# Kernel optimization log

Measured on AMD Instinct MI355X. Metric: run time of the kernel, lower is better.

The kernel has to match this reference:

```python
import jax, jax.numpy as jnp
import numpy as np

B, T, LD, PD, W, NL = 2048, 256, 32, 8, 64, 3
TH, CH = LD * 2, W * 2  # token/channel mixing hidden dims (expansion=2)


def setup_inputs() -> dict:
    key = jax.random.key(0)
    ks = jax.random.split(key, 12)
    n = lambda k, s, sc=0.02: jax.random.normal(k, s, jnp.float32) * sc
    return {
        "phys": jax.random.normal(ks[0], (B, T, PD), jnp.float32),
        "latents": jax.random.uniform(ks[1], (B, LD), jnp.float32),
        "pos_emb": n(ks[2], (1, LD, W)),
        "tokW": n(ks[3], (1, W)), "tokb": jnp.zeros((W,), jnp.float32),
        "physW1": n(ks[4], (PD, W)), "physb1": jnp.zeros((W,), jnp.float32),
        "physW2": n(ks[5], (W, W)), "physb2": jnp.zeros((W,), jnp.float32),
        "tn_g": jnp.ones((NL, W), jnp.float32), "tn_b": jnp.zeros((NL, W), jnp.float32),
        "tiW": n(ks[6], (NL, LD, TH)), "tib": jnp.zeros((NL, TH), jnp.float32),
        "toW": n(ks[7], (NL, TH, LD)), "tob": jnp.zeros((NL, LD), jnp.float32),
        "cn_g": jnp.ones((NL, W), jnp.float32), "cn_b": jnp.zeros((NL, W), jnp.float32),
        "ciW": n(ks[8], (NL, W, CH)), "cib": jnp.zeros((NL, CH), jnp.float32),
        "coW": n(ks[9], (NL, CH, W)), "cob": jnp.zeros((NL, W), jnp.float32),
        "hn_g": jnp.ones((W,), jnp.float32), "hn_b": jnp.zeros((W,), jnp.float32),
        "headW": n(ks[10], (W, 1), 0.0002),  # 0.02 init * 0.01 scaling from torch
        "headb": jnp.zeros((1,), jnp.float32),
    }


def _ln(x, g, b):
    m = jnp.mean(x, -1, keepdims=True)
    v = jnp.mean((x - m) ** 2, -1, keepdims=True)
    return (x - m) * jax.lax.rsqrt(v + 1e-5) * g + b


def reference(phys, latents, pos_emb, tokW, tokb, physW1, physb1, physW2, physb2,
              tn_g, tn_b, tiW, tib, toW, tob, cn_g, cn_b, ciW, cib, coW, cob,
              hn_g, hn_b, headW, headb):
    gelu = lambda x: jax.nn.gelu(x, approximate=False)  # torch nn.GELU default (exact)

    def step(current, phys_t):
        # token_projection of current[..., None]: Linear(1, W)
        tokens = current[:, :, None] * tokW[0] + tokb  # [B, LD, W]
        p = gelu(phys_t @ physW1 + physb1) @ physW2 + physb2  # [B, W]
        tokens = tokens + p[:, None, :] + pos_emb
        for i in range(NL):
            # token mixing: LN over width, mix across latent tokens
            mt = jnp.swapaxes(_ln(tokens, tn_g[i], tn_b[i]), 1, 2)  # [B, W, LD]
            mt = gelu(mt @ tiW[i] + tib[i]) @ toW[i] + tob[i]       # [B, W, LD]
            tokens = tokens + jnp.swapaxes(mt, 1, 2)
            # channel mixing over width
            mc = _ln(tokens, cn_g[i], cn_b[i])
            tokens = tokens + (gelu(mc @ ciW[i] + cib[i]) @ coW[i] + cob[i])
        delta = (_ln(tokens, hn_g, hn_b) @ headW + headb)[..., 0]  # [B, LD]
        new = jnp.clip(current + delta, 0.0, 1.0)
        return new, new

    _, outs = jax.lax.scan(step, latents, jnp.swapaxes(phys, 0, 1))  # [T, B, LD]
    return jnp.swapaxes(outs, 0, 1)  # [B, T, LD]
```

## Files before the change

kernel.cpp:

```cpp
#include <hip/hip_runtime.h>
#include <math.h>


namespace {
constexpr int Tt = 256, NL = 3;

typedef float    f32x4 __attribute__((ext_vector_type(4)));
typedef _Float16 half2 __attribute__((ext_vector_type(2)));
typedef _Float16 h16x4 __attribute__((ext_vector_type(4)));
typedef _Float16 h16x8 __attribute__((ext_vector_type(8)));

#define MFMA32(a, b, c) __builtin_amdgcn_mfma_f32_16x16x32_f16((a), (b), (c), 0, 0, 0)
#define MFMA16(a, b, c) __builtin_amdgcn_mfma_f32_16x16x16f16((a), (b), (c), 0, 0, 0)

__device__ __forceinline__ half2 h2c(float v) { return (half2)((_Float16)v); }
__device__ __forceinline__ f32x4 f4s(float v) { return (f32x4)v; }
__device__ __forceinline__ half2 pkrtz(float a, float b) {
    return __builtin_bit_cast(half2, __builtin_amdgcn_cvt_pkrtz(a, b));
}
__device__ __forceinline__ void st4h(short* p, half2 a, half2 b) {
    uint2 v;
    v.x = __builtin_bit_cast(unsigned int, a);
    v.y = __builtin_bit_cast(unsigned int, b);
    *(uint2*)p = v;
}
__device__ __forceinline__ h16x4 h4(half2 a, half2 b) {
    h16x4 v; v[0] = a[0]; v[1] = a[1]; v[2] = b[0]; v[3] = b[1]; return v;
}
__device__ __forceinline__ half2 gelu_pk(half2 x) {
    half2 tc = __builtin_elementwise_min(__builtin_elementwise_max(x, h2c(-3.0f)), h2c(3.0f));
    half2 s = (tc * tc) * h2c(0.125f);
    half2 p = s * h2c(0.1455169f) + h2c(-0.446340f);
    p = s * p + h2c(0.604927f);
    p = s * p + h2c(-0.529702f);
    p = s * p + h2c(0.3989423f);
    return x * (h2c(0.5f) + tc * p);
}
__device__ __forceinline__ float gelu_f(float x) {
    float tc = fminf(fmaxf(x, -3.f), 3.f);
    float s = tc * tc;
    float p = fmaf(s, 3.55266e-5f, -8.71758e-4f);
    p = fmaf(s, p, 9.45198e-3f);
    p = fmaf(s, p, -6.62128e-2f);
    p = fmaf(s, p, 0.3989423f);
    return x * fmaf(tc, p, 0.5f);
}
__device__ __forceinline__ float rowsum16(float x) {
    x += __builtin_bit_cast(float, __builtin_amdgcn_update_dpp(0, __builtin_bit_cast(int, x), 0x121, 0xf, 0xf, false));
    x += __builtin_bit_cast(float, __builtin_amdgcn_update_dpp(0, __builtin_bit_cast(int, x), 0x122, 0xf, 0xf, false));
    x += __builtin_bit_cast(float, __builtin_amdgcn_update_dpp(0, __builtin_bit_cast(int, x), 0x124, 0xf, 0xf, false));
    x += __builtin_bit_cast(float, __builtin_amdgcn_update_dpp(0, __builtin_bit_cast(int, x), 0x128, 0xf, 0xf, false));
    return x;
}
__device__ __forceinline__ short f2h(float x) {
    return __builtin_bit_cast(short, (_Float16)x);
}

__global__ void lno_prep(const float* __restrict__ tiW, const float* __restrict__ toW,
                         const float* __restrict__ ciW, const float* __restrict__ coW,
                         const float* __restrict__ physW2, short* __restrict__ wsf) {
    int id = blockIdx.x * 256 + threadIdx.x;
    if (id < 6144) {
        int e = id & 255, tile = id >> 8;
        int lane = e >> 2, j = e & 3;
        int q = lane >> 4, cc = lane & 15;
        int kc = tile & 1, u = (tile >> 1) & 3, il = tile >> 3;
        wsf[id] = f2h(tiW[il * 2048 + (16 * kc + 4 * q + j) * 64 + 16 * u + cc]);
    } else if (id < 12288) {
        int t = id - 6144;
        int e = t & 255, tile = t >> 8;
        int lane = e >> 2, j = e & 3;
        int q = lane >> 4, cc = lane & 15;
        int kc = tile & 3, mt = (tile >> 2) & 1, il = tile >> 3;
        wsf[id] = f2h(toW[il * 2048 + (16 * kc + 4 * q + j) * 32 + 16 * mt + cc]);
    } else if (id < 36864) {
        int t = id - 12288;
        int j = t & 7, lane = (t >> 3) & 63, g = t >> 9;
        int il = g >> 4, mtc = (g >> 1) & 7, ks = g & 1;
        int m = mtc * 16 + (lane & 15), k = ks * 32 + (lane >> 4) * 8 + j;
        wsf[id] = f2h(ciW[il * 8192 + k * 128 + m]);
    } else if (id < 61440) {
        int t = id - 36864;
        int j = t & 7, lane = (t >> 3) & 63, g = t >> 9;
        int il = g >> 4, nt = (g >> 2) & 3, ks = g & 3;
        int n = nt * 16 + (lane & 15), k = ks * 32 + (lane >> 4) * 8 + j;
        wsf[id] = f2h(coW[il * 8192 + k * 64 + n]);
    } else if (id < 65536) {
        int t = id - 61440;
        int w = t >> 6, k = t & 63;
        ((float*)(wsf + 61440))[t] = physW2[k * 64 + w];
    }
}

__global__ void lno_phys(const float* __restrict__ phys, const float* __restrict__ physW1,
                         const float* __restrict__ physb1, const float* __restrict__ physW2,
                         const float* __restrict__ physb2, short* __restrict__ pout) {
    __shared__ float hsh[4][64];
    const int lane = threadIdx.x & 63, wv = threadIdx.x >> 6;
    const size_t bt = (size_t)blockIdx.x * 4 + wv;
    const float* pt = phys + bt * 8;
    float4 px0 = *(const float4*)pt, px1 = *(const float4*)(pt + 4);
    float a = physb1[lane];
    a = fmaf(px0.x, physW1[0 * 64 + lane], a);
    a = fmaf(px0.y, physW1[1 * 64 + lane], a);
    a = fmaf(px0.z, physW1[2 * 64 + lane], a);
    a = fmaf(px0.w, physW1[3 * 64 + lane], a);
    a = fmaf(px1.x, physW1[4 * 64 + lane], a);
    a = fmaf(px1.y, physW1[5 * 64 + lane], a);
    a = fmaf(px1.z, physW1[6 * 64 + lane], a);
    a = fmaf(px1.w, physW1[7 * 64 + lane], a);
    hsh[wv][lane] = gelu_f(a);
    float acc = physb2[lane];
#pragma unroll
    for (int k = 0; k < 64; ++k) acc = fmaf(hsh[wv][k], physW2[k * 64 + lane], acc);
    pout[bt * 64 + (lane & 15) * 4 + (lane >> 4)] = f2h(acc);
}

__global__ __launch_bounds__(512, 1) void lno_scan(
    const float* __restrict__ latents, const float* __restrict__ pos_emb,
    const float* __restrict__ tokW,    const float* __restrict__ tokb,
    const float* __restrict__ tn_g,    const float* __restrict__ tn_b,
    const float* __restrict__ tib,     const float* __restrict__ tob,
    const float* __restrict__ cn_g,    const float* __restrict__ cn_b,
    const float* __restrict__ cib,     const float* __restrict__ cob,
    const float* __restrict__ hn_g,    const float* __restrict__ hn_b,
    const float* __restrict__ headW,   const float* __restrict__ headb,
    const short* __restrict__ wsf,     const short* pbuf, float* out)
{
    __shared__ __align__(16) short wAll[61440];
    __shared__ __align__(16) short scr[8][2048];
    __shared__ __align__(16) float biasL[1632];

    const int tid = threadIdx.x, lane = tid & 63, wv = tid >> 6;
    const int q = lane >> 4, c = lane & 15;
    const int b = blockIdx.x * 8 + wv;
    short* sc = scr[wv];

    const short* A1L = wAll;
    const short* A2L = wAll + 6144;
    const short* A3L = wAll + 12288;
    const short* B4L = wAll + 36864;

    {
        const unsigned int* src = (const unsigned int*)wsf;
#pragma unroll
        for (int i = 0; i < 15; ++i) {
            const int cid = wv * 15 + i;
            __builtin_amdgcn_global_load_lds(src + cid * 256 + lane * 4,
                                             (unsigned int*)&wAll[cid * 512], 16, 0, 0);
        }
    }
    for (int i = tid; i < 192; i += 512) {
        biasL[i] = tib[i];
        biasL[672 + i]  = tn_g[i];
        biasL[864 + i]  = tn_b[i];
        biasL[1056 + i] = cn_g[i];
        biasL[1248 + i] = cn_b[i];
        biasL[1440 + i] = cob[i];
    }
    for (int i = tid; i < 96;  i += 512) biasL[192 + i] = tob[i];
    for (int i = tid; i < 384; i += 512) biasL[288 + i] = cib[i];

    float tokw_r[4], gh_r[4];
#pragma unroll
    for (int nt = 0; nt < 4; ++nt) {
        tokw_r[nt] = tokW[nt * 16 + c];
        gh_r[nt]   = hn_g[nt * 16 + c] * headW[nt * 16 + c];
    }
    float bhp = 0.f;
#pragma unroll
    for (int nt = 0; nt < 4; ++nt) bhp = fmaf(hn_b[nt * 16 + c], headW[nt * 16 + c], bhp);
    const float bh = rowsum16(bhp) + headb[0];

    h16x4 peh[2][4];
#pragma unroll
    for (int mt = 0; mt < 2; ++mt)
#pragma unroll
        for (int r = 0; r < 4; ++r) {
            const int row = mt * 16 + q * 4 + r;
            float v0 = pos_emb[row * 64 +  0 + c] + tokb[ 0 + c];
            float v1 = pos_emb[row * 64 + 16 + c] + tokb[16 + c];
            float v2 = pos_emb[row * 64 + 32 + c] + tokb[32 + c];
            float v3 = pos_emb[row * 64 + 48 + c] + tokb[48 + c];
            peh[mt][r] = h4(pkrtz(v0, v1), pkrtz(v2, v3));
        }

    f32x4 cur8[2];
#pragma unroll
    for (int mt = 0; mt < 2; ++mt)
        cur8[mt] = *(const f32x4*)(latents + b * 32 + mt * 16 + q * 4);

    f32x4 tok[2][4];

    __syncthreads();

    auto stats = [&](f32x4 (&mean)[2], f32x4 (&rsig)[2]) {
#pragma unroll
        for (int mt = 0; mt < 2; ++mt) {
            f32x4 s4 = (tok[mt][0] + tok[mt][1]) + (tok[mt][2] + tok[mt][3]);
            f32x4 q4 = tok[mt][0] * tok[mt][0];
            q4 = __builtin_elementwise_fma(tok[mt][1], tok[mt][1], q4);
            q4 = __builtin_elementwise_fma(tok[mt][2], tok[mt][2], q4);
            q4 = __builtin_elementwise_fma(tok[mt][3], tok[mt][3], q4);
#pragma unroll
            for (int r = 0; r < 4; ++r) {
                float ss = rowsum16(s4[r]);
                float qq = rowsum16(q4[r]);
                float m = ss * 0.015625f;
                float v = fmaf(-m, m, qq * 0.015625f);
                mean[mt][r] = m;
                rsig[mt][r] = __builtin_amdgcn_rsqf(v + 1e-5f);
            }
        }
    };

    const short* pb = pbuf + (size_t)b * Tt * 64 + c * 4;
    h16x4 pvc = *(const h16x4*)pb;

#pragma unroll 1
    for (int t = 0; t < Tt; ++t) {
        const h16x4 pv = pvc;
        if (t + 1 < Tt) pvc = *(const h16x4*)(pb + (t + 1) * 64);

        {
            f32x4 pvx;
#pragma unroll
            for (int nt = 0; nt < 4; ++nt) pvx[nt] = (float)pv[nt];
#pragma unroll
            for (int mt = 0; mt < 2; ++mt)
#pragma unroll
                for (int r = 0; r < 4; ++r) {
#pragma unroll
                    for (int nt = 0; nt < 4; ++nt)
                        tok[nt == 0 ? mt : mt][nt][r] =
                            0.f;
                }
#pragma unroll
            for (int mt = 0; mt < 2; ++mt)
#pragma unroll
                for (int r = 0; r < 4; ++r) {
#pragma unroll
                    for (int nt = 0; nt < 4; ++nt)
                        tok[mt][nt][r] = fmaf(cur8[mt][r], tokw_r[nt],
                                              (float)peh[mt][r][nt] + pvx[nt]);
                }
        }

#pragma unroll
        for (int il = 0; il < NL; ++il) {
            f32x4 mean[2], rsig[2];
            stats(mean, rsig);
            h16x4 yh[2][4];
#pragma unroll
            for (int nt = 0; nt < 4; ++nt) {
                const float tng = biasL[672 + il * 64 + nt * 16 + c];
                const float tnb = biasL[864 + il * 64 + nt * 16 + c];
#pragma unroll
                for (int mt = 0; mt < 2; ++mt) {
                    f32x4 y = __builtin_elementwise_fma((tok[mt][nt] - mean[mt]) * rsig[mt],
                                                        f4s(tng), f4s(tnb));
                    yh[mt][nt] = h4(pkrtz(y[0], y[1]), pkrtz(y[2], y[3]));
                }
            }
#pragma unroll
            for (int mt = 0; mt < 2; ++mt) {
                const f32x4 tb = *(const f32x4*)&biasL[192 + il * 32 + mt * 16 + q * 4];
#pragma unroll
                for (int nt = 0; nt < 4; ++nt) tok[mt][nt] += tb;
            }
            h16x4 b2[4][4];
#pragma unroll
            for (int u = 0; u < 4; ++u) {
                const h16x4 a1k0 = *(const h16x4*)(A1L + ((il * 4 + u) * 2 + 0) * 256 + lane * 4);
                const h16x4 a1k1 = *(const h16x4*)(A1L + ((il * 4 + u) * 2 + 1) * 256 + lane * 4);
                const f32x4 bi = *(const f32x4*)&biasL[il * 64 + u * 16 + q * 4];
#pragma unroll
                for (int nt = 0; nt < 4; ++nt) {
                    f32x4 hv = MFMA16(a1k0, yh[0][nt], bi);
                    hv = MFMA16(a1k1, yh[1][nt], hv);
                    b2[u][nt] = h4(gelu_pk(pkrtz(hv[0], hv[1])),
                                   gelu_pk(pkrtz(hv[2], hv[3])));
                }
            }
#pragma unroll
            for (int mt = 0; mt < 2; ++mt)
#pragma unroll
                for (int kc = 0; kc < 4; ++kc) {
                    const h16x4 a2 = *(const h16x4*)(A2L + ((il * 2 + mt) * 4 + kc) * 256 + lane * 4);
#pragma unroll
                    for (int nt = 0; nt < 4; ++nt)
                        tok[mt][nt] = MFMA16(a2, b2[kc][nt], tok[mt][nt]);
                }

            stats(mean, rsig);
            float cng[4], cnb[4];
#pragma unroll
            for (int nt = 0; nt < 4; ++nt) {
                cng[nt] = biasL[1056 + il * 64 + nt * 16 + c];
                cnb[nt] = biasL[1248 + il * 64 + nt * 16 + c];
            }
#pragma unroll
            for (int mt = 0; mt < 2; ++mt)
#pragma unroll
                for (int nt = 0; nt < 4; ++nt) {
                    f32x4 v4 = __builtin_elementwise_fma((tok[mt][nt] - mean[mt]) * rsig[mt],
                                                         f4s(cng[nt]), f4s(cnb[nt]));
#pragma unroll
                    for (int r = 0; r < 4; ++r)
                        sc[(mt * 2 + (nt >> 1)) * 512 +
                           (q * 2 + (c >> 3) + 16 * r + 8 * (nt & 1)) * 8 + (c & 7)] = f2h(v4[r]);
                }
            h16x8 b3[4];
            {
                const int lp = ((c >> 2) * 2 + (q & 1)) + 8 * ((c & 3) * 2 + (q >> 1));
#pragma unroll
                for (int F = 0; F < 4; ++F) b3[F] = *(const h16x8*)&sc[F * 512 + lp * 8];
            }
#pragma unroll
            for (int nt = 0; nt < 4; ++nt) {
                const f32x4 cv = f4s(biasL[1440 + il * 64 + nt * 16 + c]);
#pragma unroll
                for (int mt = 0; mt < 2; ++mt) tok[mt][nt] += cv;
            }
#pragma unroll
            for (int hh = 0; hh < 2; ++hh) {
#pragma unroll
                for (int mm = 0; mm < 4; ++mm) {
                    const int mtc = hh * 4 + mm;
                    const h16x8 a30 = *(const h16x8*)(A3L + il * 8192 + (mtc * 2 + 0) * 512 + lane * 8);
                    const h16x8 a31 = *(const h16x8*)(A3L + il * 8192 + (mtc * 2 + 1) * 512 + lane * 8);
                    const f32x4 bi3 = *(const f32x4*)&biasL[288 + il * 128 + mtc * 16 + q * 4];
#pragma unroll
                    for (int ntl = 0; ntl < 2; ++ntl) {
                        f32x4 acc = MFMA32(a30, b3[ntl * 2 + 0], bi3);
                        acc = MFMA32(a31, b3[ntl * 2 + 1], acc);
                        st4h(&sc[((ntl * 2 + ((mtc >> 1) & 1)) * 64 +
                                  ((mtc & 1) * 2 + (q >> 1)) * 16 + c) * 8 + (q & 1) * 4],
                             gelu_pk(pkrtz(acc[0], acc[1])), gelu_pk(pkrtz(acc[2], acc[3])));
                    }
                }
                h16x8 a4[2][2];
#pragma unroll
                for (int mt = 0; mt < 2; ++mt)
#pragma unroll
                    for (int kk = 0; kk < 2; ++kk)
                        a4[mt][kk] = *(const h16x8*)&sc[((mt * 2 + kk) * 64 + lane) * 8];
#pragma unroll
                for (int nt = 0; nt < 4; ++nt) {
                    const h16x8 b40 = *(const h16x8*)(B4L + il * 8192 + (nt * 4 + hh * 2 + 0) * 512 + lane * 8);
                    const h16x8 b41 = *(const h16x8*)(B4L + il * 8192 + (nt * 4 + hh * 2 + 1) * 512 + lane * 8);
#pragma unroll
                    for (int mt = 0; mt < 2; ++mt) {
                        tok[mt][nt] = MFMA32(a4[mt][0], b40, tok[mt][nt]);
                        tok[mt][nt] = MFMA32(a4[mt][1], b41, tok[mt][nt]);
                    }
                }
            }
        }

        {
            f32x4 mean[2], rsig[2];
            stats(mean, rsig);
#pragma unroll
            for (int mt = 0; mt < 2; ++mt) {
                f32x4 l4 = (tok[mt][0] - mean[mt]) * f4s(gh_r[0]);
                l4 = __builtin_elementwise_fma(tok[mt][1] - mean[mt], f4s(gh_r[1]), l4);
                l4 = __builtin_elementwise_fma(tok[mt][2] - mean[mt], f4s(gh_r[2]), l4);
                l4 = __builtin_elementwise_fma(tok[mt][3] - mean[mt], f4s(gh_r[3]), l4);
                f32x4 ls;
#pragma unroll
                for (int r = 0; r < 4; ++r) ls[r] = rowsum16(l4[r]);
                f32x4 nv = cur8[mt] + __builtin_elementwise_fma(rsig[mt], ls, f4s(bh));
                nv = __builtin_elementwise_min(__builtin_elementwise_max(nv, f4s(0.f)), f4s(1.f));
                cur8[mt] = nv;
            }
            if (c == 0) {
                float* op = out + ((size_t)b * Tt + t) * 32 + q * 4;
                *(f32x4*)(op) = cur8[0];
                *(f32x4*)(op + 16) = cur8[1];
            }
        }
    }
}
}

extern "C" void kernel_launch(void* const* d_in, const int* in_sizes, int n_in,
                              void* d_out, int out_size, void* d_ws, size_t ws_size,
                              hipStream_t stream) {
    (void)in_sizes; (void)n_in; (void)ws_size; (void)out_size;
    const float* phys    = (const float*)d_in[0];
    const float* latents = (const float*)d_in[1];
    const float* pos_emb = (const float*)d_in[2];
    const float* tokW    = (const float*)d_in[3];
    const float* tokb    = (const float*)d_in[4];
    const float* physW1  = (const float*)d_in[5];
    const float* physb1  = (const float*)d_in[6];
    const float* physW2  = (const float*)d_in[7];
    const float* physb2  = (const float*)d_in[8];
    const float* tn_g    = (const float*)d_in[9];
    const float* tn_b    = (const float*)d_in[10];
    const float* tiW     = (const float*)d_in[11];
    const float* tib     = (const float*)d_in[12];
    const float* toW     = (const float*)d_in[13];
    const float* tob     = (const float*)d_in[14];
    const float* cn_g    = (const float*)d_in[15];
    const float* cn_b    = (const float*)d_in[16];
    const float* ciW     = (const float*)d_in[17];
    const float* cib     = (const float*)d_in[18];
    const float* coW     = (const float*)d_in[19];
    const float* cob     = (const float*)d_in[20];
    const float* hn_g    = (const float*)d_in[21];
    const float* hn_b    = (const float*)d_in[22];
    const float* headW   = (const float*)d_in[23];
    const float* headb   = (const float*)d_in[24];

    lno_prep<<<dim3(256), dim3(256), 0, stream>>>(tiW, toW, ciW, coW, physW2, (short*)d_ws);
    lno_phys<<<dim3(131072), dim3(256), 0, stream>>>(phys, physW1, physb1, physW2, physb2,
                                                     (short*)d_out);
    lno_scan<<<dim3(256), dim3(512), 0, stream>>>(
        latents, pos_emb, tokW, tokb, tn_g, tn_b, tib, tob,
        cn_g, cn_b, cib, cob, hn_g, hn_b, headW, headb,
        (const short*)d_ws, (const short*)d_out, (float*)d_out);
}
```

Measured before the change: 6.059 ms.

## Read scan weights from global memory and shrink blocks to four waves

```diff
diff --git a/kernel.cpp b/kernel.cpp
--- a/kernel.cpp
+++ b/kernel.cpp
@@ -116,7 +116,7 @@
     pout[bt * 64 + (lane & 15) * 4 + (lane >> 4)] = f2h(acc);
 }
 
-__global__ __launch_bounds__(512, 1) void lno_scan(
+__global__ __launch_bounds__(256, 2) void lno_scan(
     const float* __restrict__ latents, const float* __restrict__ pos_emb,
     const float* __restrict__ tokW,    const float* __restrict__ tokb,
     const float* __restrict__ tn_g,    const float* __restrict__ tn_b,
@@ -127,30 +127,20 @@
     const float* __restrict__ headW,   const float* __restrict__ headb,
     const short* __restrict__ wsf,     const short* pbuf, float* out)
 {
-    __shared__ __align__(16) short wAll[61440];
-    __shared__ __align__(16) short scr[8][2048];
+    __shared__ __align__(16) short scr[4][2048];
     __shared__ __align__(16) float biasL[1632];
 
     const int tid = threadIdx.x, lane = tid & 63, wv = tid >> 6;
     const int q = lane >> 4, c = lane & 15;
-    const int b = blockIdx.x * 8 + wv;
+    const int b = blockIdx.x * 4 + wv;
     short* sc = scr[wv];
 
-    const short* A1L = wAll;
-    const short* A2L = wAll + 6144;
-    const short* A3L = wAll + 12288;
-    const short* B4L = wAll + 36864;
-
-    {
-        const unsigned int* src = (const unsigned int*)wsf;
-#pragma unroll
-        for (int i = 0; i < 15; ++i) {
-            const int cid = wv * 15 + i;
-            __builtin_amdgcn_global_load_lds(src + cid * 256 + lane * 4,
-                                             (unsigned int*)&wAll[cid * 512], 16, 0, 0);
-        }
-    }
-    for (int i = tid; i < 192; i += 512) {
+    const short* A1G = wsf;
+    const short* A2G = wsf + 6144;
+    const short* A3G = wsf + 12288;
+    const short* B4G = wsf + 36864;
+
+    for (int i = tid; i < 192; i += 256) {
         biasL[i] = tib[i];
         biasL[672 + i]  = tn_g[i];
         biasL[864 + i]  = tn_b[i];
@@ -158,8 +148,8 @@
         biasL[1248 + i] = cn_b[i];
         biasL[1440 + i] = cob[i];
     }
-    for (int i = tid; i < 96;  i += 512) biasL[192 + i] = tob[i];
-    for (int i = tid; i < 384; i += 512) biasL[288 + i] = cib[i];
+    for (int i = tid; i < 96;  i += 256) biasL[192 + i] = tob[i];
+    for (int i = tid; i < 384; i += 256) biasL[288 + i] = cib[i];
 
     float tokw_r[4], gh_r[4];
 #pragma unroll
@@ -232,15 +222,6 @@
                 for (int r = 0; r < 4; ++r) {
 #pragma unroll
                     for (int nt = 0; nt < 4; ++nt)
-                        tok[nt == 0 ? mt : mt][nt][r] =
-                            0.f;
-                }
-#pragma unroll
-            for (int mt = 0; mt < 2; ++mt)
-#pragma unroll
-                for (int r = 0; r < 4; ++r) {
-#pragma unroll
-                    for (int nt = 0; nt < 4; ++nt)
                         tok[mt][nt][r] = fmaf(cur8[mt][r], tokw_r[nt],
                                               (float)peh[mt][r][nt] + pvx[nt]);
                 }
@@ -271,8 +252,8 @@
             h16x4 b2[4][4];
 #pragma unroll
             for (int u = 0; u < 4; ++u) {
-                const h16x4 a1k0 = *(const h16x4*)(A1L + ((il * 4 + u) * 2 + 0) * 256 + lane * 4);
-                const h16x4 a1k1 = *(const h16x4*)(A1L + ((il * 4 + u) * 2 + 1) * 256 + lane * 4);
+                const h16x4 a1k0 = *(const h16x4*)(A1G + ((il * 4 + u) * 2 + 0) * 256 + lane * 4);
+                const h16x4 a1k1 = *(const h16x4*)(A1G + ((il * 4 + u) * 2 + 1) * 256 + lane * 4);
                 const f32x4 bi = *(const f32x4*)&biasL[il * 64 + u * 16 + q * 4];
 #pragma unroll
                 for (int nt = 0; nt < 4; ++nt) {
@@ -286,7 +267,7 @@
             for (int mt = 0; mt < 2; ++mt)
 #pragma unroll
                 for (int kc = 0; kc < 4; ++kc) {
-                    const h16x4 a2 = *(const h16x4*)(A2L + ((il * 2 + mt) * 4 + kc) * 256 + lane * 4);
+                    const h16x4 a2 = *(const h16x4*)(A2G + ((il * 2 + mt) * 4 + kc) * 256 + lane * 4);
 #pragma unroll
                     for (int nt = 0; nt < 4; ++nt)
                         tok[mt][nt] = MFMA16(a2, b2[kc][nt], tok[mt][nt]);
@@ -327,8 +308,8 @@
 #pragma unroll
                 for (int mm = 0; mm < 4; ++mm) {
                     const int mtc = hh * 4 + mm;
-                    const h16x8 a30 = *(const h16x8*)(A3L + il * 8192 + (mtc * 2 + 0) * 512 + lane * 8);
-                    const h16x8 a31 = *(const h16x8*)(A3L + il * 8192 + (mtc * 2 + 1) * 512 + lane * 8);
+                    const h16x8 a30 = *(const h16x8*)(A3G + il * 8192 + (mtc * 2 + 0) * 512 + lane * 8);
+                    const h16x8 a31 = *(const h16x8*)(A3G + il * 8192 + (mtc * 2 + 1) * 512 + lane * 8);
                     const f32x4 bi3 = *(const f32x4*)&biasL[288 + il * 128 + mtc * 16 + q * 4];
 #pragma unroll
                     for (int ntl = 0; ntl < 2; ++ntl) {
@@ -347,8 +328,8 @@
                         a4[mt][kk] = *(const h16x8*)&sc[((mt * 2 + kk) * 64 + lane) * 8];
 #pragma unroll
                 for (int nt = 0; nt < 4; ++nt) {
-                    const h16x8 b40 = *(const h16x8*)(B4L + il * 8192 + (nt * 4 + hh * 2 + 0) * 512 + lane * 8);
-                    const h16x8 b41 = *(const h16x8*)(B4L + il * 8192 + (nt * 4 + hh * 2 + 1) * 512 + lane * 8);
+                    const h16x8 b40 = *(const h16x8*)(B4G + il * 8192 + (nt * 4 + hh * 2 + 0) * 512 + lane * 8);
+                    const h16x8 b41 = *(const h16x8*)(B4G + il * 8192 + (nt * 4 + hh * 2 + 1) * 512 + lane * 8);
 #pragma unroll
                     for (int mt = 0; mt < 2; ++mt) {
                         tok[mt][nt] = MFMA32(a4[mt][0], b40, tok[mt][nt]);
@@ -417,7 +398,7 @@
     lno_prep<<<dim3(256), dim3(256), 0, stream>>>(tiW, toW, ciW, coW, physW2, (short*)d_ws);
     lno_phys<<<dim3(131072), dim3(256), 0, stream>>>(phys, physW1, physb1, physW2, physb2,
                                                      (short*)d_out);
-    lno_scan<<<dim3(256), dim3(512), 0, stream>>>(
+    lno_scan<<<dim3(512), dim3(256), 0, stream>>>(
         latents, pos_emb, tokW, tokb, tn_g, tn_b, tib, tob,
         cn_g, cn_b, cib, cob, hn_g, hn_b, headW, headb,
         (const short*)d_ws, (const short*)d_out, (float*)d_out);
```

Result: slower. 10.21 ms (+68.5%).
